# Kernel tuning notes

Hardware: AMD Instinct MI355X
Metric: run time of the kernel (lower is better)

Reference implementation:

```python
import jax, jax.numpy as jnp
import numpy as np
import math
from jax import lax

VOCAB = 32000
D = 128          # embedding_dim
S = 512          # seq_len == input_channels
B = 8
HID = 512        # hidden_size
NBUCK = 32       # n_buckets
NHYP = 5         # log2(n_buckets)
ENCODERS = 2
OUT = 6
EPS = 1e-5


def _positional_encoding(max_len, d):
    pos = np.arange(max_len, dtype=np.float32)[:, None]
    div = np.exp(np.arange(0, d, 2, dtype=np.float32) * (-math.log(10000.0) / d))
    pe = np.zeros((max_len, d), dtype=np.float32)
    pe[:, 0::2] = np.sin(pos * div)
    pe[:, 1::2] = np.cos(pos * div)
    return jnp.asarray(pe)


def setup_inputs() -> dict:
    key = jax.random.key(0)
    ks = jax.random.split(key, 10)
    emb = jax.random.normal(ks[0], (VOCAB, D), jnp.float32)
    emb = emb.at[VOCAB - 1].set(0.0)  # padding_idx row is zero in torch
    sc = 0.05
    return {
        "inputs": jax.random.randint(ks[1], (B, S), 0, VOCAB - 1),
        "emb": emb,
        # Faithful quirk: pe is indexed by x.size(0)=batch, so only pe[:B] is used.
        "pe": _positional_encoding(B, D),               # [B, D]
        "hyperplanes": jax.random.normal(ks[2], (D + 1, NHYP), jnp.float32),
        "Wq": jax.random.normal(ks[3], (D, D), jnp.float32) * sc,
        "bq": jnp.zeros((D,), jnp.float32),
        "Wv": jax.random.normal(ks[4], (D, D), jnp.float32) * sc,
        "bv": jnp.zeros((D,), jnp.float32),
        "ln_g": jnp.ones((D,), jnp.float32),
        "ln_b": jnp.zeros((D,), jnp.float32),
        "W1": jax.random.normal(ks[5], (D, HID), jnp.float32) * sc,
        "b1": jnp.zeros((HID,), jnp.float32),
        "W2": jax.random.normal(ks[6], (HID, D), jnp.float32) * sc,
        "b2": jnp.zeros((D,), jnp.float32),
        "Wm": jax.random.normal(ks[7], (S * D, OUT), jnp.float32) * 0.01,
        "bm": jnp.zeros((OUT,), jnp.float32),
    }


def _layernorm(x, g, b):
    mu = jnp.mean(x, axis=-1, keepdims=True)
    var = jnp.mean(jnp.square(x - mu), axis=-1, keepdims=True)
    return (x - mu) * lax.rsqrt(var + EPS) * g + b


def _lsh_attention(x, Wq, bq, Wv, bv, hyperplanes):
    q = x @ Wq + bq                                      # [B,S,D]
    v = x @ Wv + bv                                      # [B,S,D]
    # LSH bucket ids from q (hard threshold -> no grad through buckets)
    qh = jnp.concatenate([q, jnp.ones(q.shape[:-1] + (1,), q.dtype)], axis=-1)
    proj = jnp.einsum('bse,en->bsn', qh, hyperplanes)    # [B,S,NHYP]
    bits = (proj >= 0).astype(jnp.float32)
    pow2 = 2.0 ** jnp.arange(NHYP, dtype=jnp.float32)
    buckets = jnp.einsum('bsn,n->bs', bits, pow2).astype(jnp.int32)  # [B,S]
    scale = 1.0 / math.sqrt(D)

    def step(acc, i):
        # Faithful quirk: masked_fill zeros tokens IN bucket i (inverted mask).
        keep = (buckets != i)[..., None]                 # [B,S,1]
        qb = jnp.where(keep, q, 0.0)
        vb = jnp.where(keep, v, 0.0)
        att = jax.nn.softmax(jnp.einsum('bsd,btd->bst', qb, qb) * scale, axis=-1)
        return acc + jnp.einsum('bst,btd->bsd', att, vb), None

    out, _ = lax.scan(step, jnp.zeros_like(x), jnp.arange(NBUCK))
    return out


def reference(inputs, emb, pe, hyperplanes, Wq, bq, Wv, bv, ln_g, ln_b,
              W1, b1, W2, b2, Wm, bm):
    x = emb[inputs]                                      # [B,S,D]
    x = x + pe[:, None, :]                               # broadcast over seq (faithful quirk)
    for _ in range(ENCODERS):
        a = _lsh_attention(x, Wq, bq, Wv, bv, hyperplanes)
        x = _layernorm(a, ln_g, ln_b)
        x = (jax.nn.relu(x @ W1 + b1) @ W2 + b2) + x     # fc residual (dropout=eval)
        x = _layernorm(x, ln_g, ln_b)
    x = x.reshape(x.shape[0], -1)                        # [B, S*D]
    return x @ Wm + bm                                   # [B, OUT]
```

## Files before the change

### kernel.cpp

```cpp
#include <hip/hip_runtime.h>
#include <hip/hip_bf16.h>

#define BB   8
#define SS   512
#define DD   128
#define HH   512
#define NBK  32


__global__ void k_embed(const int* __restrict__ idx, const float* __restrict__ emb,
                        const float* __restrict__ pe, float* __restrict__ x) {
    int b = blockIdx.x;
    int t = b * 16384 + blockIdx.y * 256 + threadIdx.x;
    int tok = t >> 5, d4 = (t & 31) * 4;
    float4 ev = *(const float4*)&emb[(size_t)idx[tok] * DD + d4];
    float4 pv = *(const float4*)&pe[b * DD + d4];
    ev.x += pv.x; ev.y += pv.y; ev.z += pv.z; ev.w += pv.w;
    *(float4*)&x[(size_t)tok * DD + d4] = ev;
}

__global__ __launch_bounds__(256) void k_qvb(const float* __restrict__ x,
        const float* __restrict__ Wq, const float* __restrict__ bq,
        const float* __restrict__ Wv, const float* __restrict__ bv,
        const float* __restrict__ hyp,
        float* __restrict__ q, float* __restrict__ v, float* __restrict__ qT,
        int* __restrict__ bucket) {
    int rb = blockIdx.x * 32 + blockIdx.y;
    __shared__ __align__(16) float xs[16][132];
    __shared__ float qts[128][17];
    int tid = threadIdx.x;
    #pragma unroll
    for (int it = 0; it < 2; ++it) {
        int lin = tid + 256 * it;
        int r = lin >> 5, kq = (lin & 31) * 4;
        *(float4*)&xs[r][kq] = *(const float4*)&x[(size_t)(rb * 16 + r) * DD + kq];
    }
    __syncthreads();
    int tx = tid & 63;
    int ty = tid >> 6;
    float2 aq[4], av[4];
    #pragma unroll
    for (int i = 0; i < 4; ++i) { aq[i] = make_float2(0.f, 0.f); av[i] = make_float2(0.f, 0.f); }
    for (int g = 0; g < 32; ++g) {
        int kb = g * 4;
        float4 a0 = *(const float4*)&xs[ty * 4 + 0][kb];
        float4 a1 = *(const float4*)&xs[ty * 4 + 1][kb];
        float4 a2 = *(const float4*)&xs[ty * 4 + 2][kb];
        float4 a3 = *(const float4*)&xs[ty * 4 + 3][kb];
        #pragma unroll
        for (int j = 0; j < 4; ++j) {
            float2 wq = *(const float2*)&Wq[(size_t)(kb + j) * DD + tx * 2];
            float2 wv = *(const float2*)&Wv[(size_t)(kb + j) * DD + tx * 2];
            float c0 = (j == 0) ? a0.x : (j == 1) ? a0.y : (j == 2) ? a0.z : a0.w;
            float c1 = (j == 0) ? a1.x : (j == 1) ? a1.y : (j == 2) ? a1.z : a1.w;
            float c2 = (j == 0) ? a2.x : (j == 1) ? a2.y : (j == 2) ? a2.z : a2.w;
            float c3 = (j == 0) ? a3.x : (j == 1) ? a3.y : (j == 2) ? a3.z : a3.w;
            aq[0].x += c0 * wq.x; aq[0].y += c0 * wq.y; av[0].x += c0 * wv.x; av[0].y += c0 * wv.y;
            aq[1].x += c1 * wq.x; aq[1].y += c1 * wq.y; av[1].x += c1 * wv.x; av[1].y += c1 * wv.y;
            aq[2].x += c2 * wq.x; aq[2].y += c2 * wq.y; av[2].x += c2 * wv.x; av[2].y += c2 * wv.y;
            aq[3].x += c3 * wq.x; aq[3].y += c3 * wq.y; av[3].x += c3 * wv.x; av[3].y += c3 * wv.y;
        }
    }
    float2 bqv = *(const float2*)&bq[tx * 2];
    float2 bvv = *(const float2*)&bv[tx * 2];
    float2 oq[4], ov[4];
    #pragma unroll
    for (int i = 0; i < 4; ++i) {
        oq[i] = make_float2(aq[i].x + bqv.x, aq[i].y + bqv.y);
        ov[i] = make_float2(av[i].x + bvv.x, av[i].y + bvv.y);
        int row = rb * 16 + ty * 4 + i;
        *(float2*)&q[(size_t)row * DD + tx * 2] = oq[i];
        *(float2*)&v[(size_t)row * DD + tx * 2] = ov[i];
        qts[2 * tx][ty * 4 + i]     = oq[i].x;
        qts[2 * tx + 1][ty * 4 + i] = oq[i].y;
    }
    float h0[5], h1[5];
    #pragma unroll
    for (int h = 0; h < 5; ++h) {
        h0[h] = hyp[(2 * tx) * 5 + h];
        h1[h] = hyp[(2 * tx + 1) * 5 + h];
    }
    float pr[4][5];
    #pragma unroll
    for (int r = 0; r < 4; ++r)
        #pragma unroll
        for (int h = 0; h < 5; ++h)
            pr[r][h] = oq[r].x * h0[h] + oq[r].y * h1[h];
    #pragma unroll
    for (int o = 1; o < 64; o <<= 1)
        #pragma unroll
        for (int r = 0; r < 4; ++r)
            #pragma unroll
            for (int h = 0; h < 5; ++h)
                pr[r][h] += __shfl_xor(pr[r][h], o, 64);
    if (tx == 0) {
        #pragma unroll
        for (int r = 0; r < 4; ++r) {
            int bb = 0;
            #pragma unroll
            for (int h = 0; h < 5; ++h)
                if (pr[r][h] + hyp[128 * 5 + h] >= 0.f) bb |= (1 << h);
            bucket[rb * 16 + ty * 4 + r] = bb;
        }
    }
    __syncthreads();
    {
        int b  = blockIdx.x;
        int t0 = blockIdx.y * 16;
        int k  = tid >> 1, o = (tid & 1) * 8;
        float4 v0 = make_float4(qts[k][o], qts[k][o + 1], qts[k][o + 2], qts[k][o + 3]);
        float4 v1 = make_float4(qts[k][o + 4], qts[k][o + 5], qts[k][o + 6], qts[k][o + 7]);
        size_t base = ((size_t)b * DD + k) * SS + t0 + o;
        *(float4*)&qT[base]     = v0;
        *(float4*)&qT[base + 4] = v1;
    }
}

__global__ __launch_bounds__(256) void k_vb(const float* __restrict__ v,
        const int* __restrict__ bucket, float* __restrict__ Vb,
        int* __restrict__ cnt) {
    int b  = blockIdx.x;
    int bk = blockIdx.y;
    int tid = threadIdx.x;
    __shared__ int bkt_sh[512];
    __shared__ float red[128];
    bkt_sh[tid]       = bucket[b * SS + tid];
    bkt_sh[tid + 256] = bucket[b * SS + tid + 256];
    __syncthreads();
    int d = tid & 127, half = tid >> 7;
    const float* vbp = v + (size_t)b * SS * DD + d;
    float acc = 0.f;
    #pragma unroll 8
    for (int i = 0; i < 256; ++i) {
        int tok = half * 256 + i;
        float val = vbp[(size_t)tok * DD];
        acc += (bkt_sh[tok] == bk) ? val : 0.f;
    }
    if (half == 1) red[d] = acc;
    __syncthreads();
    if (half == 0)
        Vb[(size_t)((b << 5) + bk) * DD + d] = acc + red[d];
    if (tid < 64) {
        int c = 0;
        #pragma unroll
        for (int i = 0; i < 8; ++i) c += (bkt_sh[tid * 8 + i] == bk) ? 1 : 0;
        #pragma unroll
        for (int o = 1; o < 64; o <<= 1) c += __shfl_xor(c, o, 64);
        if (tid == 0) cnt[(b << 5) + bk] = c;
    }
}

__global__ __launch_bounds__(512) void k_gattn(const float* __restrict__ qT,
        const float* __restrict__ q, const float* __restrict__ v,
        const int* __restrict__ bucket, const int* __restrict__ cnt,
        const float* __restrict__ Vb,
        const float* __restrict__ g, const float* __restrict__ lb,
        float* __restrict__ x) {
    int bz = blockIdx.x, s0 = blockIdx.y * 16;
    int tid = threadIdx.x;
    __shared__ __align__(16) float qs[16][132];
    __shared__ __align__(16) float cs[16][528];
    __shared__ __align__(16) float osh[16][132];
    __shared__ int   bkt[512];
    __shared__ float Wsh[16][32];
    __shared__ float rsh[16][32];
    __shared__ float Zsh[16], Rsh[16], Msh[16];
    __shared__ float cntf[32];
    __shared__ int   bssh[16];
    {
        int r = tid >> 5, kq = (tid & 31) * 4;
        *(float4*)&qs[r][kq] = *(const float4*)&q[(size_t)(bz * SS + s0 + r) * DD + kq];
    }
    bkt[tid] = bucket[bz * SS + tid];
    if (tid < 32) cntf[tid] = (float)cnt[(bz << 5) + tid];
    if (tid < 16) bssh[tid] = bucket[bz * SS + s0 + tid];
    __syncthreads();
    const float scale = 0.088388347648318447f;
    {
        int cc  = tid >> 7;
        int ty  = (tid >> 5) & 3;
        int txg = tid & 31;
        float4 acc[4];
        #pragma unroll
        for (int i = 0; i < 4; ++i) acc[i] = make_float4(0.f, 0.f, 0.f, 0.f);
        const float* qtb = qT + (size_t)bz * DD * SS + cc * 128 + txg * 4;
        for (int gg = 0; gg < 32; ++gg) {
            int kb = gg * 4;
            float4 a0 = *(const float4*)&qs[ty * 4 + 0][kb];
            float4 a1 = *(const float4*)&qs[ty * 4 + 1][kb];
            float4 a2 = *(const float4*)&qs[ty * 4 + 2][kb];
            float4 a3 = *(const float4*)&qs[ty * 4 + 3][kb];
            #pragma unroll
            for (int j = 0; j < 4; ++j) {
                float4 b4 = *(const float4*)&qtb[(size_t)(kb + j) * SS];
                float c0 = (j == 0) ? a0.x : (j == 1) ? a0.y : (j == 2) ? a0.z : a0.w;
                float c1 = (j == 0) ? a1.x : (j == 1) ? a1.y : (j == 2) ? a1.z : a1.w;
                float c2 = (j == 0) ? a2.x : (j == 1) ? a2.y : (j == 2) ? a2.z : a2.w;
                float c3 = (j == 0) ? a3.x : (j == 1) ? a3.y : (j == 2) ? a3.z : a3.w;
                acc[0].x += c0 * b4.x; acc[0].y += c0 * b4.y; acc[0].z += c0 * b4.z; acc[0].w += c0 * b4.w;
                acc[1].x += c1 * b4.x; acc[1].y += c1 * b4.y; acc[1].z += c1 * b4.z; acc[1].w += c1 * b4.w;
                acc[2].x += c2 * b4.x; acc[2].y += c2 * b4.y; acc[2].z += c2 * b4.z; acc[2].w += c2 * b4.w;
                acc[3].x += c3 * b4.x; acc[3].y += c3 * b4.y; acc[3].z += c3 * b4.z; acc[3].w += c3 * b4.w;
            }
        }
        #pragma unroll
        for (int i = 0; i < 4; ++i) {
            float4 p;
            p.x = acc[i].x * scale; p.y = acc[i].y * scale;
            p.z = acc[i].z * scale; p.w = acc[i].w * scale;
            *(float4*)&cs[ty * 4 + i][cc * 128 + txg * 4] = p;
        }
    }
    __syncthreads();
    int row = tid >> 5, l = tid & 31;
    {
        float m = 0.f;
        #pragma unroll
        for (int i = 0; i < 16; ++i) m = fmaxf(m, cs[row][l + 32 * i]);
        #pragma unroll
        for (int o = 1; o < 32; o <<= 1) m = fmaxf(m, __shfl_xor(m, o, 32));
        if (l == 0) Msh[row] = m;
        Wsh[row][l] = 0.f;
    }
    __syncthreads();
    {
        float Ms = Msh[row];
        #pragma unroll
        for (int i = 0; i < 16; ++i) {
            int c = l + 32 * i;
            float ev = __expf(cs[row][c] - Ms);
            cs[row][c] = ev;
            atomicAdd(&Wsh[row][bkt[c]], ev);
        }
    }
    __syncthreads();
    if (tid < 16) {
        float z = 0.f;
        #pragma unroll
        for (int i = 0; i < NBK; ++i) z += Wsh[tid][i];
        Zsh[tid] = z;
    }
    __syncthreads();
    rsh[row][l] = 1.0f / (Zsh[row] - Wsh[row][l] + cntf[l] * __expf(-Msh[row]));
    __syncthreads();
    if (tid < 16) {
        int bs = bssh[tid];
        float R = 0.f;
        #pragma unroll
        for (int i = 0; i < NBK; ++i) R += (i == bs) ? 0.f : rsh[tid][i];
        Rsh[tid] = R;
    }
    __syncthreads();
    {
        float R = Rsh[row];
        int bs = bssh[row];
        #pragma unroll
        for (int i = 0; i < 16; ++i) {
            int c = l + 32 * i;
            int bc = bkt[c];
            float rsel = (bc == bs) ? 0.f : rsh[row][bc];
            cs[row][c] *= (R - rsel);
        }
    }
    __syncthreads();
    {
        int kh = tid >> 7;
        int ty = (tid >> 5) & 3;
        int tx = tid & 31;
        float4 acc[4];
        #pragma unroll
        for (int i = 0; i < 4; ++i) acc[i] = make_float4(0.f, 0.f, 0.f, 0.f);
        const float* vb_base = v + (size_t)bz * SS * DD + tx * 4;
        for (int gg = 0; gg < 32; ++gg) {
            int kb = kh * 128 + gg * 4;
            float4 a0 = *(const float4*)&cs[ty * 4 + 0][kb];
            float4 a1 = *(const float4*)&cs[ty * 4 + 1][kb];
            float4 a2 = *(const float4*)&cs[ty * 4 + 2][kb];
            float4 a3 = *(const float4*)&cs[ty * 4 + 3][kb];
            #pragma unroll
            for (int j = 0; j < 4; ++j) {
                float4 vj = *(const float4*)&vb_base[(size_t)(kb + j) * DD];
                float c0 = (j == 0) ? a0.x : (j == 1) ? a0.y : (j == 2) ? a0.z : a0.w;
                float c1 = (j == 0) ? a1.x : (j == 1) ? a1.y : (j == 2) ? a1.z : a1.w;
                float c2 = (j == 0) ? a2.x : (j == 1) ? a2.y : (j == 2) ? a2.z : a2.w;
                float c3 = (j == 0) ? a3.x : (j == 1) ? a3.y : (j == 2) ? a3.z : a3.w;
                acc[0].x += c0 * vj.x; acc[0].y += c0 * vj.y; acc[0].z += c0 * vj.z; acc[0].w += c0 * vj.w;
                acc[1].x += c1 * vj.x; acc[1].y += c1 * vj.y; acc[1].z += c1 * vj.z; acc[1].w += c1 * vj.w;
                acc[2].x += c2 * vj.x; acc[2].y += c2 * vj.y; acc[2].z += c2 * vj.z; acc[2].w += c2 * vj.w;
                acc[3].x += c3 * vj.x; acc[3].y += c3 * vj.y; acc[3].z += c3 * vj.z; acc[3].w += c3 * vj.w;
            }
        }
        if (kh == 3) {
            #pragma unroll
            for (int i = 0; i < 4; ++i)
                *(float4*)&osh[ty * 4 + i][tx * 4] = acc[i];
        }
        __syncthreads();
        #pragma unroll
        for (int p = 2; p >= 1; --p) {
            if (kh == p) {
                #pragma unroll
                for (int i = 0; i < 4; ++i) {
                    int r = ty * 4 + i;
                    float4 o = *(const float4*)&osh[r][tx * 4];
                    o.x += acc[i].x; o.y += acc[i].y; o.z += acc[i].z; o.w += acc[i].w;
                    *(float4*)&osh[r][tx * 4] = o;
                }
            }
            __syncthreads();
        }
        if (kh == 0) {
            float4 vs = make_float4(0.f, 0.f, 0.f, 0.f);
            #pragma unroll
            for (int i = 0; i < NBK; ++i) {
                float4 t = *(const float4*)&Vb[(size_t)((bz << 5) + i) * DD + tx * 4];
                vs.x += t.x; vs.y += t.y; vs.z += t.z; vs.w += t.w;
            }
            const float inv512 = 1.0f / 512.0f;
            #pragma unroll
            for (int i = 0; i < 4; ++i) {
                int r = ty * 4 + i;
                int bs = bssh[r];
                float4 vb4 = *(const float4*)&Vb[(size_t)((bz << 5) + bs) * DD + tx * 4];
                float4 p = *(const float4*)&osh[r][tx * 4];
                p.x += acc[i].x + (vs.x - vb4.x) * inv512;
                p.y += acc[i].y + (vs.y - vb4.y) * inv512;
                p.z += acc[i].z + (vs.z - vb4.z) * inv512;
                p.w += acc[i].w + (vs.w - vb4.w) * inv512;
                *(float4*)&osh[r][tx * 4] = p;
            }
        }
    }
    __syncthreads();
    {
        float4 val = *(const float4*)&osh[row][l * 4];
        float s = val.x + val.y + val.z + val.w;
        float ss = val.x * val.x + val.y * val.y + val.z * val.z + val.w * val.w;
        #pragma unroll
        for (int o = 1; o < 32; o <<= 1) {
            s  += __shfl_xor(s, o, 32);
            ss += __shfl_xor(ss, o, 32);
        }
        float mean = s * (1.f / 128.f);
        float var = ss * (1.f / 128.f) - mean * mean;
        float rstd = rsqrtf(var + 1e-5f);
        float4 gv = *(const float4*)&g[l * 4];
        float4 bv = *(const float4*)&lb[l * 4];
        float4 out;
        out.x = (val.x - mean) * rstd * gv.x + bv.x;
        out.y = (val.y - mean) * rstd * gv.y + bv.y;
        out.z = (val.z - mean) * rstd * gv.z + bv.z;
        out.w = (val.w - mean) * rstd * gv.w + bv.w;
        *(float4*)&x[(size_t)(bz * SS + s0 + row) * DD + l * 4] = out;
    }
}

__global__ __launch_bounds__(512) void k_ffn(const float* __restrict__ x,
        const float* __restrict__ W1, const float* __restrict__ b1,
        const float* __restrict__ W2, const float* __restrict__ b2,
        const float* __restrict__ g, const float* __restrict__ lb,
        float* __restrict__ xout) {
    int rb = blockIdx.x * 32 + blockIdx.y;
    int tid = threadIdx.x;
    __shared__ __align__(16) float xs[16][132];
    __shared__ __align__(16) float hs[16][520];
    __shared__ __align__(16) float osh[16][132];
    {
        int r = tid >> 5, kq = (tid & 31) * 4;
        *(float4*)&xs[r][kq] = *(const float4*)&x[(size_t)(rb * 16 + r) * DD + kq];
    }
    __syncthreads();
    {
        int tx = tid & 127, ty = tid >> 7;
        float4 acc[4];
        #pragma unroll
        for (int i = 0; i < 4; ++i) acc[i] = make_float4(0.f, 0.f, 0.f, 0.f);
        for (int gg = 0; gg < 32; ++gg) {
            int kb = gg * 4;
            float4 a0 = *(const float4*)&xs[ty * 4 + 0][kb];
            float4 a1 = *(const float4*)&xs[ty * 4 + 1][kb];
            float4 a2 = *(const float4*)&xs[ty * 4 + 2][kb];
            float4 a3 = *(const float4*)&xs[ty * 4 + 3][kb];
            #pragma unroll
            for (int j = 0; j < 4; ++j) {
                float4 w = *(const float4*)&W1[(size_t)(kb + j) * HH + tx * 4];
                float c0 = (j == 0) ? a0.x : (j == 1) ? a0.y : (j == 2) ? a0.z : a0.w;
                float c1 = (j == 0) ? a1.x : (j == 1) ? a1.y : (j == 2) ? a1.z : a1.w;
                float c2 = (j == 0) ? a2.x : (j == 1) ? a2.y : (j == 2) ? a2.z : a2.w;
                float c3 = (j == 0) ? a3.x : (j == 1) ? a3.y : (j == 2) ? a3.z : a3.w;
                acc[0].x += c0 * w.x; acc[0].y += c0 * w.y; acc[0].z += c0 * w.z; acc[0].w += c0 * w.w;
                acc[1].x += c1 * w.x; acc[1].y += c1 * w.y; acc[1].z += c1 * w.z; acc[1].w += c1 * w.w;
                acc[2].x += c2 * w.x; acc[2].y += c2 * w.y; acc[2].z += c2 * w.z; acc[2].w += c2 * w.w;
                acc[3].x += c3 * w.x; acc[3].y += c3 * w.y; acc[3].z += c3 * w.z; acc[3].w += c3 * w.w;
            }
        }
        float4 bi = *(const float4*)&b1[tx * 4];
        #pragma unroll
        for (int i = 0; i < 4; ++i) {
            float4 hv;
            hv.x = fmaxf(acc[i].x + bi.x, 0.f);
            hv.y = fmaxf(acc[i].y + bi.y, 0.f);
            hv.z = fmaxf(acc[i].z + bi.z, 0.f);
            hv.w = fmaxf(acc[i].w + bi.w, 0.f);
            *(float4*)&hs[ty * 4 + i][tx * 4] = hv;
        }
    }
    __syncthreads();
    {
        int kh = tid >> 7;
        int ty = (tid >> 5) & 3;
        int tx = tid & 31;
        float4 acc[4];
        #pragma unroll
        for (int i = 0; i < 4; ++i) acc[i] = make_float4(0.f, 0.f, 0.f, 0.f);
        for (int gg = 0; gg < 32; ++gg) {
            int kb = kh * 128 + gg * 4;
            float4 a0 = *(const float4*)&hs[ty * 4 + 0][kb];
            float4 a1 = *(const float4*)&hs[ty * 4 + 1][kb];
            float4 a2 = *(const float4*)&hs[ty * 4 + 2][kb];
            float4 a3 = *(const float4*)&hs[ty * 4 + 3][kb];
            #pragma unroll
            for (int j = 0; j < 4; ++j) {
                float4 w = *(const float4*)&W2[(size_t)(kb + j) * DD + tx * 4];
                float c0 = (j == 0) ? a0.x : (j == 1) ? a0.y : (j == 2) ? a0.z : a0.w;
                float c1 = (j == 0) ? a1.x : (j == 1) ? a1.y : (j == 2) ? a1.z : a1.w;
                float c2 = (j == 0) ? a2.x : (j == 1) ? a2.y : (j == 2) ? a2.z : a2.w;
                float c3 = (j == 0) ? a3.x : (j == 1) ? a3.y : (j == 2) ? a3.z : a3.w;
                acc[0].x += c0 * w.x; acc[0].y += c0 * w.y; acc[0].z += c0 * w.z; acc[0].w += c0 * w.w;
                acc[1].x += c1 * w.x; acc[1].y += c1 * w.y; acc[1].z += c1 * w.z; acc[1].w += c1 * w.w;
                acc[2].x += c2 * w.x; acc[2].y += c2 * w.y; acc[2].z += c2 * w.z; acc[2].w += c2 * w.w;
                acc[3].x += c3 * w.x; acc[3].y += c3 * w.y; acc[3].z += c3 * w.z; acc[3].w += c3 * w.w;
            }
        }
        if (kh == 0) {
            float4 bi = *(const float4*)&b2[tx * 4];
            #pragma unroll
            for (int i = 0; i < 4; ++i) {
                int r = ty * 4 + i;
                float4 res = *(const float4*)&xs[r][tx * 4];
                float4 o;
                o.x = acc[i].x + bi.x + res.x;
                o.y = acc[i].y + bi.y + res.y;
                o.z = acc[i].z + bi.z + res.z;
                o.w = acc[i].w + bi.w + res.w;
                *(float4*)&osh[r][tx * 4] = o;
            }
        }
        __syncthreads();
        #pragma unroll
        for (int p = 1; p < 4; ++p) {
            if (kh == p) {
                #pragma unroll
                for (int i = 0; i < 4; ++i) {
                    int r = ty * 4 + i;
                    float4 o = *(const float4*)&osh[r][tx * 4];
                    o.x += acc[i].x; o.y += acc[i].y; o.z += acc[i].z; o.w += acc[i].w;
                    *(float4*)&osh[r][tx * 4] = o;
                }
            }
            __syncthreads();
        }
    }
    int row = tid >> 5, l = tid & 31;
    float4 val = *(const float4*)&osh[row][l * 4];
    float s = val.x + val.y + val.z + val.w;
    float ss = val.x * val.x + val.y * val.y + val.z * val.z + val.w * val.w;
    #pragma unroll
    for (int o = 1; o < 32; o <<= 1) {
        s  += __shfl_xor(s, o, 32);
        ss += __shfl_xor(ss, o, 32);
    }
    float mean = s * (1.f / 128.f);
    float var = ss * (1.f / 128.f) - mean * mean;
    float rstd = rsqrtf(var + 1e-5f);
    float4 gv = *(const float4*)&g[l * 4];
    float4 bv = *(const float4*)&lb[l * 4];
    float4 out;
    out.x = (val.x - mean) * rstd * gv.x + bv.x;
    out.y = (val.y - mean) * rstd * gv.y + bv.y;
    out.z = (val.z - mean) * rstd * gv.z + bv.z;
    out.w = (val.w - mean) * rstd * gv.w + bv.w;
    *(float4*)&xout[(size_t)(rb * 16 + row) * DD + l * 4] = out;
}

__global__ __launch_bounds__(256) void k_final(const float* __restrict__ x,
        const float* __restrict__ Wm, const float* __restrict__ bm,
        float* __restrict__ out) {
    int b = blockIdx.x >> 5, chunk = blockIdx.x & 31;
    int tid = threadIdx.x;
    const float* xr = x + (size_t)b * 65536 + chunk * 2048;
    const float* wr = Wm + (size_t)(chunk * 2048) * 6;
    float p[6] = {0.f, 0.f, 0.f, 0.f, 0.f, 0.f};
    #pragma unroll
    for (int it = 0; it < 8; ++it) {
        int j = tid + 256 * it;
        float xv = xr[j];
        const float* w = wr + (size_t)j * 6;
        p[0] += xv * w[0]; p[1] += xv * w[1]; p[2] += xv * w[2];
        p[3] += xv * w[3]; p[4] += xv * w[4]; p[5] += xv * w[5];
    }
    #pragma unroll
    for (int o = 0; o < 6; ++o)
        #pragma unroll
        for (int off = 1; off < 64; off <<= 1)
            p[o] += __shfl_xor(p[o], off, 64);
    __shared__ float red[4][6];
    int wv = tid >> 6;
    if ((tid & 63) == 0)
        #pragma unroll
        for (int o = 0; o < 6; ++o) red[wv][o] = p[o];
    __syncthreads();
    if (tid < 6) {
        float sv = red[0][tid] + red[1][tid] + red[2][tid] + red[3][tid];
        if (chunk == 0) sv += bm[tid];
        atomicAdd(&out[b * 6 + tid], sv);
    }
}

extern "C" void kernel_launch(void* const* d_in, const int* in_sizes, int n_in,
                              void* d_out, int out_size, void* d_ws, size_t ws_size,
                              hipStream_t stream) {
    const int*   inputs = (const int*)  d_in[0];
    const float* emb    = (const float*)d_in[1];
    const float* pe     = (const float*)d_in[2];
    const float* hyp    = (const float*)d_in[3];
    const float* Wq     = (const float*)d_in[4];
    const float* bq     = (const float*)d_in[5];
    const float* Wv     = (const float*)d_in[6];
    const float* bv     = (const float*)d_in[7];
    const float* ln_g   = (const float*)d_in[8];
    const float* ln_b   = (const float*)d_in[9];
    const float* W1     = (const float*)d_in[10];
    const float* b1     = (const float*)d_in[11];
    const float* W2     = (const float*)d_in[12];
    const float* b2     = (const float*)d_in[13];
    const float* Wm     = (const float*)d_in[14];
    const float* bm     = (const float*)d_in[15];

    float* F = (float*)d_ws;
    float* x     = F + 0;
    float* q     = F + 524288;
    float* v     = F + 1048576;
    float* qT    = F + 1572864;
    float* Vb    = F + 2097152;
    int*   cnt   = (int*)(F + 2129920);
    int*   bucket= (int*)(F + 2130176);

    hipMemsetAsync(d_out, 0, (size_t)out_size * 4, stream);
    k_embed<<<dim3(8, 64), 256, 0, stream>>>(inputs, emb, pe, x);

    for (int enc = 0; enc < 2; ++enc) {
        k_qvb<<<dim3(8, 32), 256, 0, stream>>>(x, Wq, bq, Wv, bv, hyp, q, v, qT, bucket);
        k_vb<<<dim3(8, 32), 256, 0, stream>>>(v, bucket, Vb, cnt);
        k_gattn<<<dim3(8, 32), 512, 0, stream>>>(qT, q, v, bucket, cnt, Vb, ln_g, ln_b, x);
        k_ffn<<<dim3(8, 32), 512, 0, stream>>>(x, W1, b1, W2, b2, ln_g, ln_b, x);
    }
    k_final<<<48 * 32 / 6, 256, 0, stream>>>(x, Wm, bm, (float*)d_out);
}
```

Measured before the change: 262.5 us.

## Retile per-block GEMMs so each global weight load feeds eight rows

The four small GEMMs inside the attention and FFN kernels (q·qT scores, P·V, x·W1, h·W2) are remapped so each thread accumulates 8 rows instead of 4. The shared K dimension is split across thread halves or quarters, with partial sums reduced through shared memory. Each global float4 or float2 load of qT, V, W1 and W2 is now reused across more rows, cutting global and L2 traffic per FMA. In exchange there are extra shared-memory reduction passes and barriers, plus higher register pressure from 8 accumulators and 8 cached A vectors.

```diff
diff --git a/kernel.cpp b/kernel.cpp
--- a/kernel.cpp
+++ b/kernel.cpp
@@ -174,44 +174,52 @@
     bkt[tid] = bucket[bz * SS + tid];
     if (tid < 32) cntf[tid] = (float)cnt[(bz << 5) + tid];
     if (tid < 16) bssh[tid] = bucket[bz * SS + s0 + tid];
+    Wsh[tid >> 5][tid & 31] = 0.f;
     __syncthreads();
     const float scale = 0.088388347648318447f;
     {
-        int cc  = tid >> 7;
-        int ty  = (tid >> 5) & 3;
-        int txg = tid & 31;
-        float4 acc[4];
-        #pragma unroll
-        for (int i = 0; i < 4; ++i) acc[i] = make_float4(0.f, 0.f, 0.f, 0.f);
-        const float* qtb = qT + (size_t)bz * DD * SS + cc * 128 + txg * 4;
-        for (int gg = 0; gg < 32; ++gg) {
-            int kb = gg * 4;
-            float4 a0 = *(const float4*)&qs[ty * 4 + 0][kb];
-            float4 a1 = *(const float4*)&qs[ty * 4 + 1][kb];
-            float4 a2 = *(const float4*)&qs[ty * 4 + 2][kb];
-            float4 a3 = *(const float4*)&qs[ty * 4 + 3][kb];
+        int kh   = tid >> 8;
+        int rg   = (tid >> 7) & 1;
+        int slot = tid & 127;
+        float4 acc[8];
+        #pragma unroll
+        for (int i = 0; i < 8; ++i) acc[i] = make_float4(0.f, 0.f, 0.f, 0.f);
+        const float* qtb = qT + (size_t)bz * DD * SS + (size_t)kh * 64 * SS + slot * 4;
+        for (int gg = 0; gg < 16; ++gg) {
+            int kb = kh * 64 + gg * 4;
+            float4 a[8];
+            #pragma unroll
+            for (int i = 0; i < 8; ++i) a[i] = *(const float4*)&qs[rg * 8 + i][kb];
             #pragma unroll
             for (int j = 0; j < 4; ++j) {
-                float4 b4 = *(const float4*)&qtb[(size_t)(kb + j) * SS];
-                float c0 = (j == 0) ? a0.x : (j == 1) ? a0.y : (j == 2) ? a0.z : a0.w;
-                float c1 = (j == 0) ? a1.x : (j == 1) ? a1.y : (j == 2) ? a1.z : a1.w;
-                float c2 = (j == 0) ? a2.x : (j == 1) ? a2.y : (j == 2) ? a2.z : a2.w;
-                float c3 = (j == 0) ? a3.x : (j == 1) ? a3.y : (j == 2) ? a3.z : a3.w;
-                acc[0].x += c0 * b4.x; acc[0].y += c0 * b4.y; acc[0].z += c0 * b4.z; acc[0].w += c0 * b4.w;
-                acc[1].x += c1 * b4.x; acc[1].y += c1 * b4.y; acc[1].z += c1 * b4.z; acc[1].w += c1 * b4.w;
-                acc[2].x += c2 * b4.x; acc[2].y += c2 * b4.y; acc[2].z += c2 * b4.z; acc[2].w += c2 * b4.w;
-                acc[3].x += c3 * b4.x; acc[3].y += c3 * b4.y; acc[3].z += c3 * b4.z; acc[3].w += c3 * b4.w;
-            }
-        }
-        #pragma unroll
-        for (int i = 0; i < 4; ++i) {
-            float4 p;
-            p.x = acc[i].x * scale; p.y = acc[i].y * scale;
-            p.z = acc[i].z * scale; p.w = acc[i].w * scale;
-            *(float4*)&cs[ty * 4 + i][cc * 128 + txg * 4] = p;
-        }
-    }
-    __syncthreads();
+                float4 b4 = *(const float4*)&qtb[(size_t)(gg * 4 + j) * SS];
+                #pragma unroll
+                for (int i = 0; i < 8; ++i) {
+                    float c = (j == 0) ? a[i].x : (j == 1) ? a[i].y : (j == 2) ? a[i].z : a[i].w;
+                    acc[i].x += c * b4.x; acc[i].y += c * b4.y;
+                    acc[i].z += c * b4.z; acc[i].w += c * b4.w;
+                }
+            }
+        }
+        if (kh == 1) {
+            #pragma unroll
+            for (int i = 0; i < 8; ++i)
+                *(float4*)&cs[rg * 8 + i][slot * 4] = acc[i];
+        }
+        __syncthreads();
+        if (kh == 0) {
+            #pragma unroll
+            for (int i = 0; i < 8; ++i) {
+                float4 p = *(const float4*)&cs[rg * 8 + i][slot * 4];
+                p.x = (p.x + acc[i].x) * scale;
+                p.y = (p.y + acc[i].y) * scale;
+                p.z = (p.z + acc[i].z) * scale;
+                p.w = (p.w + acc[i].w) * scale;
+                *(float4*)&cs[rg * 8 + i][slot * 4] = p;
+            }
+        }
+        __syncthreads();
+    }
     int row = tid >> 5, l = tid & 31;
     {
         float m = 0.f;
@@ -220,7 +228,6 @@
         #pragma unroll
         for (int o = 1; o < 32; o <<= 1) m = fmaxf(m, __shfl_xor(m, o, 32));
         if (l == 0) Msh[row] = m;
-        Wsh[row][l] = 0.f;
     }
     __syncthreads();
     {
@@ -265,73 +272,66 @@
     __syncthreads();
     {
         int kh = tid >> 7;
-        int ty = (tid >> 5) & 3;
-        int tx = tid & 31;
-        float4 acc[4];
-        #pragma unroll
-        for (int i = 0; i < 4; ++i) acc[i] = make_float4(0.f, 0.f, 0.f, 0.f);
-        const float* vb_base = v + (size_t)bz * SS * DD + tx * 4;
+        int rg = (tid >> 6) & 1;
+        int cp = tid & 63;
+        float2 acc[8];
+        #pragma unroll
+        for (int i = 0; i < 8; ++i) acc[i] = make_float2(0.f, 0.f);
+        const float* vb_base = v + (size_t)bz * SS * DD + cp * 2;
         for (int gg = 0; gg < 32; ++gg) {
             int kb = kh * 128 + gg * 4;
-            float4 a0 = *(const float4*)&cs[ty * 4 + 0][kb];
-            float4 a1 = *(const float4*)&cs[ty * 4 + 1][kb];
-            float4 a2 = *(const float4*)&cs[ty * 4 + 2][kb];
-            float4 a3 = *(const float4*)&cs[ty * 4 + 3][kb];
+            float4 a[8];
+            #pragma unroll
+            for (int i = 0; i < 8; ++i) a[i] = *(const float4*)&cs[rg * 8 + i][kb];
             #pragma unroll
             for (int j = 0; j < 4; ++j) {
-                float4 vj = *(const float4*)&vb_base[(size_t)(kb + j) * DD];
-                float c0 = (j == 0) ? a0.x : (j == 1) ? a0.y : (j == 2) ? a0.z : a0.w;
-                float c1 = (j == 0) ? a1.x : (j == 1) ? a1.y : (j == 2) ? a1.z : a1.w;
-                float c2 = (j == 0) ? a2.x : (j == 1) ? a2.y : (j == 2) ? a2.z : a2.w;
-                float c3 = (j == 0) ? a3.x : (j == 1) ? a3.y : (j == 2) ? a3.z : a3.w;
-                acc[0].x += c0 * vj.x; acc[0].y += c0 * vj.y; acc[0].z += c0 * vj.z; acc[0].w += c0 * vj.w;
-                acc[1].x += c1 * vj.x; acc[1].y += c1 * vj.y; acc[1].z += c1 * vj.z; acc[1].w += c1 * vj.w;
-                acc[2].x += c2 * vj.x; acc[2].y += c2 * vj.y; acc[2].z += c2 * vj.z; acc[2].w += c2 * vj.w;
-                acc[3].x += c3 * vj.x; acc[3].y += c3 * vj.y; acc[3].z += c3 * vj.z; acc[3].w += c3 * vj.w;
+                float2 v2 = *(const float2*)&vb_base[(size_t)(kb + j) * DD];
+                #pragma unroll
+                for (int i = 0; i < 8; ++i) {
+                    float c = (j == 0) ? a[i].x : (j == 1) ? a[i].y : (j == 2) ? a[i].z : a[i].w;
+                    acc[i].x += c * v2.x; acc[i].y += c * v2.y;
+                }
             }
         }
         if (kh == 3) {
             #pragma unroll
-            for (int i = 0; i < 4; ++i)
-                *(float4*)&osh[ty * 4 + i][tx * 4] = acc[i];
+            for (int i = 0; i < 8; ++i)
+                *(float2*)&osh[rg * 8 + i][cp * 2] = acc[i];
         }
         __syncthreads();
         #pragma unroll
         for (int p = 2; p >= 1; --p) {
             if (kh == p) {
                 #pragma unroll
-                for (int i = 0; i < 4; ++i) {
-                    int r = ty * 4 + i;
-                    float4 o = *(const float4*)&osh[r][tx * 4];
-                    o.x += acc[i].x; o.y += acc[i].y; o.z += acc[i].z; o.w += acc[i].w;
-                    *(float4*)&osh[r][tx * 4] = o;
+                for (int i = 0; i < 8; ++i) {
+                    float2 o = *(const float2*)&osh[rg * 8 + i][cp * 2];
+                    o.x += acc[i].x; o.y += acc[i].y;
+                    *(float2*)&osh[rg * 8 + i][cp * 2] = o;
                 }
             }
             __syncthreads();
         }
         if (kh == 0) {
-            float4 vs = make_float4(0.f, 0.f, 0.f, 0.f);
+            float2 vs = make_float2(0.f, 0.f);
             #pragma unroll
             for (int i = 0; i < NBK; ++i) {
-                float4 t = *(const float4*)&Vb[(size_t)((bz << 5) + i) * DD + tx * 4];
-                vs.x += t.x; vs.y += t.y; vs.z += t.z; vs.w += t.w;
+                float2 t = *(const float2*)&Vb[(size_t)((bz << 5) + i) * DD + cp * 2];
+                vs.x += t.x; vs.y += t.y;
             }
             const float inv512 = 1.0f / 512.0f;
             #pragma unroll
-            for (int i = 0; i < 4; ++i) {
-                int r = ty * 4 + i;
+            for (int i = 0; i < 8; ++i) {
+                int r = rg * 8 + i;
                 int bs = bssh[r];
-                float4 vb4 = *(const float4*)&Vb[(size_t)((bz << 5) + bs) * DD + tx * 4];
-                float4 p = *(const float4*)&osh[r][tx * 4];
-                p.x += acc[i].x + (vs.x - vb4.x) * inv512;
-                p.y += acc[i].y + (vs.y - vb4.y) * inv512;
-                p.z += acc[i].z + (vs.z - vb4.z) * inv512;
-                p.w += acc[i].w + (vs.w - vb4.w) * inv512;
-                *(float4*)&osh[r][tx * 4] = p;
-            }
-        }
-    }
-    __syncthreads();
+                float2 vb2 = *(const float2*)&Vb[(size_t)((bz << 5) + bs) * DD + cp * 2];
+                float2 p = *(const float2*)&osh[r][cp * 2];
+                p.x += acc[i].x + (vs.x - vb2.x) * inv512;
+                p.y += acc[i].y + (vs.y - vb2.y) * inv512;
+                *(float2*)&osh[r][cp * 2] = p;
+            }
+        }
+        __syncthreads();
+    }
     {
         float4 val = *(const float4*)&osh[row][l * 4];
         float s = val.x + val.y + val.z + val.w;
@@ -371,95 +371,101 @@
     }
     __syncthreads();
     {
-        int tx = tid & 127, ty = tid >> 7;
-        float4 acc[4];
-        #pragma unroll
-        for (int i = 0; i < 4; ++i) acc[i] = make_float4(0.f, 0.f, 0.f, 0.f);
-        for (int gg = 0; gg < 32; ++gg) {
-            int kb = gg * 4;
-            float4 a0 = *(const float4*)&xs[ty * 4 + 0][kb];
-            float4 a1 = *(const float4*)&xs[ty * 4 + 1][kb];
-            float4 a2 = *(const float4*)&xs[ty * 4 + 2][kb];
-            float4 a3 = *(const float4*)&xs[ty * 4 + 3][kb];
+        int kh   = tid >> 8;
+        int rg   = (tid >> 7) & 1;
+        int slot = tid & 127;
+        float4 acc[8];
+        #pragma unroll
+        for (int i = 0; i < 8; ++i) acc[i] = make_float4(0.f, 0.f, 0.f, 0.f);
+        for (int gg = 0; gg < 16; ++gg) {
+            int kb = kh * 64 + gg * 4;
+            float4 a[8];
+            #pragma unroll
+            for (int i = 0; i < 8; ++i) a[i] = *(const float4*)&xs[rg * 8 + i][kb];
             #pragma unroll
             for (int j = 0; j < 4; ++j) {
-                float4 w = *(const float4*)&W1[(size_t)(kb + j) * HH + tx * 4];
-                float c0 = (j == 0) ? a0.x : (j == 1) ? a0.y : (j == 2) ? a0.z : a0.w;
-                float c1 = (j == 0) ? a1.x : (j == 1) ? a1.y : (j == 2) ? a1.z : a1.w;
-                float c2 = (j == 0) ? a2.x : (j == 1) ? a2.y : (j == 2) ? a2.z : a2.w;
-                float c3 = (j == 0) ? a3.x : (j == 1) ? a3.y : (j == 2) ? a3.z : a3.w;
-                acc[0].x += c0 * w.x; acc[0].y += c0 * w.y; acc[0].z += c0 * w.z; acc[0].w += c0 * w.w;
-                acc[1].x += c1 * w.x; acc[1].y += c1 * w.y; acc[1].z += c1 * w.z; acc[1].w += c1 * w.w;
-                acc[2].x += c2 * w.x; acc[2].y += c2 * w.y; acc[2].z += c2 * w.z; acc[2].w += c2 * w.w;
-                acc[3].x += c3 * w.x; acc[3].y += c3 * w.y; acc[3].z += c3 * w.z; acc[3].w += c3 * w.w;
-            }
-        }
-        float4 bi = *(const float4*)&b1[tx * 4];
-        #pragma unroll
-        for (int i = 0; i < 4; ++i) {
-            float4 hv;
-            hv.x = fmaxf(acc[i].x + bi.x, 0.f);
-            hv.y = fmaxf(acc[i].y + bi.y, 0.f);
-            hv.z = fmaxf(acc[i].z + bi.z, 0.f);
-            hv.w = fmaxf(acc[i].w + bi.w, 0.f);
-            *(float4*)&hs[ty * 4 + i][tx * 4] = hv;
-        }
-    }
-    __syncthreads();
+                float4 w = *(const float4*)&W1[(size_t)(kb + j) * HH + slot * 4];
+                #pragma unroll
+                for (int i = 0; i < 8; ++i) {
+                    float c = (j == 0) ? a[i].x : (j == 1) ? a[i].y : (j == 2) ? a[i].z : a[i].w;
+                    acc[i].x += c * w.x; acc[i].y += c * w.y;
+                    acc[i].z += c * w.z; acc[i].w += c * w.w;
+                }
+            }
+        }
+        if (kh == 1) {
+            #pragma unroll
+            for (int i = 0; i < 8; ++i)
+                *(float4*)&hs[rg * 8 + i][slot * 4] = acc[i];
+        }
+        __syncthreads();
+        if (kh == 0) {
+            float4 bi = *(const float4*)&b1[slot * 4];
+            #pragma unroll
+            for (int i = 0; i < 8; ++i) {
+                float4 p = *(const float4*)&hs[rg * 8 + i][slot * 4];
+                p.x = fmaxf(p.x + acc[i].x + bi.x, 0.f);
+                p.y = fmaxf(p.y + acc[i].y + bi.y, 0.f);
+                p.z = fmaxf(p.z + acc[i].z + bi.z, 0.f);
+                p.w = fmaxf(p.w + acc[i].w + bi.w, 0.f);
+                *(float4*)&hs[rg * 8 + i][slot * 4] = p;
+            }
+        }
+        __syncthreads();
+    }
     {
         int kh = tid >> 7;
-        int ty = (tid >> 5) & 3;
-        int tx = tid & 31;
-        float4 acc[4];
-        #pragma unroll
-        for (int i = 0; i < 4; ++i) acc[i] = make_float4(0.f, 0.f, 0.f, 0.f);
+        int rg = (tid >> 6) & 1;
+        int cp = tid & 63;
+        float2 acc[8];
+        #pragma unroll
+        for (int i = 0; i < 8; ++i) acc[i] = make_float2(0.f, 0.f);
         for (int gg = 0; gg < 32; ++gg) {
             int kb = kh * 128 + gg * 4;
-            float4 a0 = *(const float4*)&hs[ty * 4 + 0][kb];
-            float4 a1 = *(const float4*)&hs[ty * 4 + 1][kb];
-            float4 a2 = *(const float4*)&hs[ty * 4 + 2][kb];
-            float4 a3 = *(const float4*)&hs[ty * 4 + 3][kb];
+            float4 a[8];
+            #pragma unroll
+            for (int i = 0; i < 8; ++i) a[i] = *(const float4*)&hs[rg * 8 + i][kb];
             #pragma unroll
             for (int j = 0; j < 4; ++j) {
-                float4 w = *(const float4*)&W2[(size_t)(kb + j) * DD + tx * 4];
-                float c0 = (j == 0) ? a0.x : (j == 1) ? a0.y : (j == 2) ? a0.z : a0.w;
-                float c1 = (j == 0) ? a1.x : (j == 1) ? a1.y : (j == 2) ? a1.z : a1.w;
-                float c2 = (j == 0) ? a2.x : (j == 1) ? a2.y : (j == 2) ? a2.z : a2.w;
-                float c3 = (j == 0) ? a3.x : (j == 1) ? a3.y : (j == 2) ? a3.z : a3.w;
-                acc[0].x += c0 * w.x; acc[0].y += c0 * w.y; acc[0].z += c0 * w.z; acc[0].w += c0 * w.w;
-                acc[1].x += c1 * w.x; acc[1].y += c1 * w.y; acc[1].z += c1 * w.z; acc[1].w += c1 * w.w;
-                acc[2].x += c2 * w.x; acc[2].y += c2 * w.y; acc[2].z += c2 * w.z; acc[2].w += c2 * w.w;
-                acc[3].x += c3 * w.x; acc[3].y += c3 * w.y; acc[3].z += c3 * w.z; acc[3].w += c3 * w.w;
-            }
-        }
-        if (kh == 0) {
-            float4 bi = *(const float4*)&b2[tx * 4];
-            #pragma unroll
-            for (int i = 0; i < 4; ++i) {
-                int r = ty * 4 + i;
-                float4 res = *(const float4*)&xs[r][tx * 4];
-                float4 o;
-                o.x = acc[i].x + bi.x + res.x;
-                o.y = acc[i].y + bi.y + res.y;
-                o.z = acc[i].z + bi.z + res.z;
-                o.w = acc[i].w + bi.w + res.w;
-                *(float4*)&osh[r][tx * 4] = o;
-            }
-        }
-        __syncthreads();
-        #pragma unroll
-        for (int p = 1; p < 4; ++p) {
+                float2 w2 = *(const float2*)&W2[(size_t)(kb + j) * DD + cp * 2];
+                #pragma unroll
+                for (int i = 0; i < 8; ++i) {
+                    float c = (j == 0) ? a[i].x : (j == 1) ? a[i].y : (j == 2) ? a[i].z : a[i].w;
+                    acc[i].x += c * w2.x; acc[i].y += c * w2.y;
+                }
+            }
+        }
+        if (kh == 3) {
+            #pragma unroll
+            for (int i = 0; i < 8; ++i)
+                *(float2*)&osh[rg * 8 + i][cp * 2] = acc[i];
+        }
+        __syncthreads();
+        #pragma unroll
+        for (int p = 2; p >= 1; --p) {
             if (kh == p) {
                 #pragma unroll
-                for (int i = 0; i < 4; ++i) {
-                    int r = ty * 4 + i;
-                    float4 o = *(const float4*)&osh[r][tx * 4];
-                    o.x += acc[i].x; o.y += acc[i].y; o.z += acc[i].z; o.w += acc[i].w;
-                    *(float4*)&osh[r][tx * 4] = o;
+                for (int i = 0; i < 8; ++i) {
+                    float2 o = *(const float2*)&osh[rg * 8 + i][cp * 2];
+                    o.x += acc[i].x; o.y += acc[i].y;
+                    *(float2*)&osh[rg * 8 + i][cp * 2] = o;
                 }
             }
             __syncthreads();
         }
+        if (kh == 0) {
+            float2 bi = *(const float2*)&b2[cp * 2];
+            #pragma unroll
+            for (int i = 0; i < 8; ++i) {
+                int r = rg * 8 + i;
+                float2 res = *(const float2*)&xs[r][cp * 2];
+                float2 p = *(const float2*)&osh[r][cp * 2];
+                p.x += acc[i].x + bi.x + res.x;
+                p.y += acc[i].y + bi.y + res.y;
+                *(float2*)&osh[r][cp * 2] = p;
+            }
+        }
+        __syncthreads();
     }
     int row = tid >> 5, l = tid & 31;
     float4 val = *(const float4*)&osh[row][l * 4];
```

Result: faster. 249.0 us (-5.1%).
